# Kernel optimization log

Hardware: AMD Instinct MI355X
Metric: run time of the kernel (lower is better)

Reference implementation:

```python
import jax, jax.numpy as jnp
import numpy as np

N, K, D = 500_000, 256, 64  # points, prototypes, feature dim


def setup_inputs() -> dict:
    key = jax.random.key(0)
    kx, km = jax.random.split(key)
    X = jax.random.normal(kx, (N, D), dtype=jnp.float32)
    mus = jax.random.normal(km, (K, D), dtype=jnp.float32)
    return {"X": X, "mus": mus}


def reference(X, mus):
    # Faithful to vmap(lambda x: argmin(sum((mus - x)**2, axis=1)))(X),
    # but expressed with the Gram-matrix distance trick so the K*D broadcast
    # is a single GEMM instead of an O(N,K,D) elementwise intermediate.
    x_sq = jnp.sum(X * X, axis=1, keepdims=True)        # [N, 1]
    mu_sq = jnp.sum(mus * mus, axis=1)                  # [K]
    d2 = x_sq - 2.0 * (X @ mus.T) + mu_sq[None, :]      # [N, K] squared dists
    return jnp.argmin(d2, axis=1)                       # [N] int assignments
```

## Files before the change

kernel.cpp:

```cpp
#include <hip/hip_runtime.h>


#define DIM 64
#define NPROTO 256
#define NBLK 512
#define GSZ 16
#define MARGIN_ACC 0.017f

using f32x4 = __attribute__((ext_vector_type(4))) float;
using f16x8 = __attribute__((ext_vector_type(8))) _Float16;

__device__ __forceinline__ f16x8 cvt8(float4 a, float4 b) {
    f16x8 r;
    r[0] = (_Float16)a.x; r[1] = (_Float16)a.y;
    r[2] = (_Float16)a.z; r[3] = (_Float16)a.w;
    r[4] = (_Float16)b.x; r[5] = (_Float16)b.y;
    r[6] = (_Float16)b.z; r[7] = (_Float16)b.w;
    return r;
}

__attribute__((amdgpu_waves_per_eu(2, 4)))
__global__ void __launch_bounds__(256)
argmin_mfma_kernel(const float* __restrict__ X,
                   const float* __restrict__ mus,
                   int* __restrict__ out,
                   unsigned* __restrict__ ws_count,
                   int* __restrict__ ws_list,
                   int use_list, int n) {
    __shared__ __align__(16) float s_seed[NPROTO];

    const int tid = threadIdx.x;
    const int w = tid >> 6;
    const int l = tid & 63;
    const int lp = l & 15;
    const int lg = l >> 4;

    f16x8 ah[16][2];
#pragma unroll
    for (int p = 0; p < 16; ++p) {
        const float* src = mus + (size_t)(p * 16 + lp) * DIM + lg * 8;
        const float4 a = *(const float4*)(src);
        const float4 b = *(const float4*)(src + 4);
        const float4 c = *(const float4*)(src + 32);
        const float4 d = *(const float4*)(src + 36);
        ah[p][0] = cvt8(a, b);
        ah[p][1] = cvt8(c, d);
        float s = 0.f;
        s = fmaf(a.x, a.x, fmaf(a.y, a.y, fmaf(a.z, a.z, fmaf(a.w, a.w, s))));
        s = fmaf(b.x, b.x, fmaf(b.y, b.y, fmaf(b.z, b.z, fmaf(b.w, b.w, s))));
        s = fmaf(c.x, c.x, fmaf(c.y, c.y, fmaf(c.z, c.z, fmaf(c.w, c.w, s))));
        s = fmaf(d.x, d.x, fmaf(d.y, d.y, fmaf(d.z, d.z, fmaf(d.w, d.w, s))));
        s += __shfl_xor(s, 16);
        s += __shfl_xor(s, 32);
        if (w == 0 && lg == 0) s_seed[p * 16 + lp] = -0.5f * s;
    }
    __syncthreads();

    const int ngroups = (n + GSZ - 1) / GSZ;
    const int NW = NBLK * 4;
    const int gwid = blockIdx.x * 4 + w;
    const int q = ngroups / NW, rr = ngroups % NW;
    const int g0 = gwid * q + (gwid < rr ? gwid : rr);
    const int cnt = q + (gwid < rr ? 1 : 0);

    const int kofs = 255 - lg * 4;

    float4 xr0, xr1, xr2, xr3;
    if (cnt > 0) {
        int row = g0 * GSZ + lp; row = (row < n) ? row : (n - 1);
        const float* rp = X + (size_t)row * DIM + lg * 8;
        xr0 = *(const float4*)(rp);
        xr1 = *(const float4*)(rp + 4);
        xr2 = *(const float4*)(rp + 32);
        xr3 = *(const float4*)(rp + 36);
    }

    for (int it = 0; it < cnt; ++it) {
        const int g = g0 + it;
        const bool more = (it + 1 < cnt);

        const f16x8 bx0 = cvt8(xr0, xr1);
        const f16x8 bx1 = cvt8(xr2, xr3);

        if (more) {
            int row = (g + 1) * GSZ + lp; row = (row < n) ? row : (n - 1);
            const float* rp = X + (size_t)row * DIM + lg * 8;
            xr0 = *(const float4*)(rp);
            xr1 = *(const float4*)(rp + 4);
            xr2 = *(const float4*)(rp + 32);
            xr3 = *(const float4*)(rp + 36);
        }

        float b1 = -3.4e38f, b2 = -3.4e38f;
#pragma unroll
        for (int p = 0; p < 16; ++p) {
            const f32x4 seed = *(const f32x4*)&s_seed[p * 16 + lg * 4];
            f32x4 acc = __builtin_amdgcn_mfma_f32_16x16x32_f16(
                ah[p][0], bx0, seed, 0, 0, 0);
            acc = __builtin_amdgcn_mfma_f32_16x16x32_f16(ah[p][1], bx1, acc,
                                                         0, 0, 0);
            float pv[4];
#pragma unroll
            for (int r = 0; r < 4; ++r) {
                unsigned u = __float_as_uint(acc[r]);
                u = (u & 0xFFFFFF00u) + (unsigned)(kofs - p * 16 - r);
                pv[r] = __uint_as_float(u);
            }
            const float t1a = fmaxf(pv[0], pv[1]), t2a = fminf(pv[0], pv[1]);
            const float t1b = fmaxf(pv[2], pv[3]), t2b = fminf(pv[2], pv[3]);
            const float p1 = fmaxf(t1a, t1b);
            const float p2 = fmaxf(fminf(t1a, t1b), fmaxf(t2a, t2b));
            const float nb2 = fmaxf(fminf(b1, p1), fmaxf(b2, p2));
            b1 = fmaxf(b1, p1);
            b2 = nb2;
        }
#pragma unroll
        for (int m = 16; m <= 32; m <<= 1) {
            const float o1 = __shfl_xor(b1, m);
            const float o2 = __shfl_xor(b2, m);
            const float nb2 = fmaxf(fminf(b1, o1), fmaxf(b2, o2));
            b1 = fmaxf(b1, o1);
            b2 = nb2;
        }

        bool fl = false;
        const int i = g * GSZ + l;
        if (l < GSZ && i < n) {
            const unsigned u1 = __float_as_uint(b1);
            const int k1 = 255 - (int)(u1 & 0xFFu);
            const float f1 = __uint_as_float(u1 & 0xFFFFFF00u);
            const float f2 =
                __uint_as_float(__float_as_uint(b2) & 0xFFFFFF00u);
            const bool close = (f1 - f2) < MARGIN_ACC;
            if (use_list) {
                out[i] = k1;
                fl = close;
            } else {
                out[i] = (int)((unsigned)k1 | (close ? 0x80000000u : 0u));
            }
        }
        if (use_list) {
            const unsigned long long mask = __ballot(fl);
            if (mask) {
                unsigned base = 0;
                if (l == 0)
                    base = atomicAdd(ws_count, (unsigned)__popcll(mask));
                base = __shfl(base, 0);
                if (fl)
                    ws_list[base + __popcll(mask & ((1ull << l) - 1))] = i;
            }
        }
    }
}

#define MSTRIDE 65

__global__ void __launch_bounds__(256)
fixup_lds_kernel(const float* __restrict__ X, const float* __restrict__ mus,
                 const unsigned* __restrict__ ws_count,
                 const int* __restrict__ ws_list, int* __restrict__ out) {
    __shared__ float s_mu[NPROTO * MSTRIDE];
    __shared__ float s_msq[NPROTO];

    const int tid = threadIdx.x;
    {
        const float4* mr = (const float4*)(mus + (size_t)tid * DIM);
        float q0 = 0.f, q1 = 0.f, q2 = 0.f, q3 = 0.f;
#pragma unroll
        for (int qq = 0; qq < 16; ++qq) {
            const float4 mv = mr[qq];
            const int base = tid * MSTRIDE + qq * 4;
            s_mu[base]     = mv.x;
            s_mu[base + 1] = mv.y;
            s_mu[base + 2] = mv.z;
            s_mu[base + 3] = mv.w;
            q0 = fmaf(mv.x, mv.x, q0);
            q1 = fmaf(mv.y, mv.y, q1);
            q2 = fmaf(mv.z, mv.z, q2);
            q3 = fmaf(mv.w, mv.w, q3);
        }
        s_msq[tid] = (q0 + q1) + (q2 + q3);
    }
    __syncthreads();

    const int l = tid & 63;
    const int gw = (int)((blockIdx.x * blockDim.x + tid) >> 6);
    const int NW = (int)((gridDim.x * blockDim.x) >> 6);
    const int nf = (int)*ws_count;

    for (int j = gw; j < nf; j += NW) {
        const int pt = ws_list[j];
        const float4* xr = (const float4*)(X + (size_t)pt * DIM);
        float4 xv[16];
        float a0 = 0.f, a1 = 0.f, a2 = 0.f, a3 = 0.f;
#pragma unroll
        for (int qq = 0; qq < 16; ++qq) {
            xv[qq] = xr[qq];
            a0 = fmaf(xv[qq].x, xv[qq].x, a0);
            a1 = fmaf(xv[qq].y, xv[qq].y, a1);
            a2 = fmaf(xv[qq].z, xv[qq].z, a2);
            a3 = fmaf(xv[qq].w, xv[qq].w, a3);
        }
        const float xsq = (a0 + a1) + (a2 + a3);
        float b1 = 3.4e38f;
        int k1 = 0;
#pragma unroll
        for (int e = 0; e < 4; ++e) {
            const int p = e * 64 + l;
            const float* mr = &s_mu[p * MSTRIDE];
            float d0 = 0.f, d1 = 0.f, d2 = 0.f, d3 = 0.f;
#pragma unroll
            for (int qq = 0; qq < 16; ++qq) {
                d0 = fmaf(mr[qq * 4],     xv[qq].x, d0);
                d1 = fmaf(mr[qq * 4 + 1], xv[qq].y, d1);
                d2 = fmaf(mr[qq * 4 + 2], xv[qq].z, d2);
                d3 = fmaf(mr[qq * 4 + 3], xv[qq].w, d3);
            }
            const float dot = (d0 + d1) + (d2 + d3);
            const float dd = (xsq - 2.0f * dot) + s_msq[p];
            if (dd < b1) { b1 = dd; k1 = p; }
        }
#pragma unroll
        for (int mm = 1; mm < 64; mm <<= 1) {
            const float ob = __shfl_xor(b1, mm);
            const int ok = __shfl_xor(k1, mm);
            if (ob < b1 || (ob == b1 && ok < k1)) { b1 = ob; k1 = ok; }
        }
        if (l == 0) out[pt] = k1;
    }
}

__device__ __forceinline__ int recompute_point(const float* __restrict__ X,
                                               const float* __restrict__ mus,
                                               int pt, int l) {
    const float4* xr = (const float4*)(X + (size_t)pt * DIM);
    float4 xv[16];
    float xa0 = 0.f, xa1 = 0.f, xa2 = 0.f, xa3 = 0.f;
#pragma unroll
    for (int qq = 0; qq < 16; ++qq) {
        xv[qq] = xr[qq];
        xa0 = fmaf(xv[qq].x, xv[qq].x, xa0);
        xa1 = fmaf(xv[qq].y, xv[qq].y, xa1);
        xa2 = fmaf(xv[qq].z, xv[qq].z, xa2);
        xa3 = fmaf(xv[qq].w, xv[qq].w, xa3);
    }
    const float xsq = (xa0 + xa1) + (xa2 + xa3);
    float b1 = 3.4e38f; int k1 = 0;
#pragma unroll
    for (int e = 0; e < 4; ++e) {
        const int p = l * 4 + e;
        const float4* mr = (const float4*)(mus + (size_t)p * DIM);
        float d0 = 0.f, d1 = 0.f, d2a = 0.f, d3 = 0.f;
        float q0 = 0.f, q1 = 0.f, q2 = 0.f, q3 = 0.f;
#pragma unroll
        for (int qq = 0; qq < 16; ++qq) {
            const float4 mv = mr[qq];
            d0 = fmaf(mv.x, xv[qq].x, d0);
            d1 = fmaf(mv.y, xv[qq].y, d1);
            d2a = fmaf(mv.z, xv[qq].z, d2a);
            d3 = fmaf(mv.w, xv[qq].w, d3);
            q0 = fmaf(mv.x, mv.x, q0);
            q1 = fmaf(mv.y, mv.y, q1);
            q2 = fmaf(mv.z, mv.z, q2);
            q3 = fmaf(mv.w, mv.w, q3);
        }
        const float dot = (d0 + d1) + (d2a + d3);
        const float msq = (q0 + q1) + (q2 + q3);
        const float dd = (xsq - 2.0f * dot) + msq;
        if (dd < b1) { b1 = dd; k1 = p; }
    }
#pragma unroll
    for (int mm = 1; mm < 64; mm <<= 1) {
        const float ob = __shfl_xor(b1, mm);
        const int ok = __shfl_xor(k1, mm);
        if (ob < b1 || (ob == b1 && ok < k1)) { b1 = ob; k1 = ok; }
    }
    return k1;
}

__global__ void __launch_bounds__(256)
fixup_scan_kernel(const float* __restrict__ X, const float* __restrict__ mus,
                  int* __restrict__ out, int n) {
    const int gw = (int)((blockIdx.x * blockDim.x + threadIdx.x) >> 6);
    const int l = threadIdx.x & 63;
    const int NW = (int)((gridDim.x * blockDim.x) >> 6);
    const int chunk = (n + NW - 1) / NW;
    const int base = gw * chunk;
    const int end = (base + chunk < n) ? (base + chunk) : n;
    for (int s = base; s < end; s += 64) {
        const int i = s + l;
        const int v = (i < end) ? out[i] : 0;
        const bool flg = (i < end) && ((unsigned)v & 0x80000000u);
        unsigned long long m = __ballot(flg);
        while (m) {
            const int src = (int)__ffsll((unsigned long long)m) - 1;
            m &= m - 1;
            const int pt = __shfl(i, src);
            const int k1 = recompute_point(X, mus, pt, l);
            if (l == 0) out[pt] = k1;
        }
    }
}

extern "C" void kernel_launch(void* const* d_in, const int* in_sizes, int n_in,
                              void* d_out, int out_size, void* d_ws, size_t ws_size,
                              hipStream_t stream) {
    const float* X = (const float*)d_in[0];
    const float* mus = (const float*)d_in[1];
    int* out = (int*)d_out;
    const int n = in_sizes[0] / DIM;

    unsigned* ws_count = (unsigned*)d_ws;
    int* ws_list = (int*)((char*)d_ws + 16);
    const int use_list = (ws_size >= 16 + (size_t)n * 4) ? 1 : 0;

    if (use_list) {
        hipMemsetAsync(d_ws, 0, 16, stream);
    }

    argmin_mfma_kernel<<<NBLK, 256, 0, stream>>>(X, mus, out, ws_count,
                                                 ws_list, use_list, n);
    if (use_list) {
        fixup_lds_kernel<<<512, 256, 0, stream>>>(X, mus, ws_count, ws_list,
                                                  out);
    } else {
        fixup_scan_kernel<<<512, 256, 0, stream>>>(X, mus, out, n);
    }
}
```

Before: 89.73 us.

## Split prototypes across two waves and process two point tiles per iteration

Blocks shrink to two waves. Each wave now holds only 128 of the prototypes in registers instead of all 256, and it processes 32 points per iteration as two 16-point MFMA tiles. The two waves exchange their partial top-2 results through LDS behind a custom barrier that waits only on LDS and leaves outstanding global prefetches in flight. This halves per-wave register pressure for the prototype fragments and raises MFMA independence, which can help occupancy and latency hiding. In exchange it adds a block barrier on every iteration and a cross-wave LDS merge.

```diff
diff --git a/kernel.cpp b/kernel.cpp
--- a/kernel.cpp
+++ b/kernel.cpp
@@ -3,8 +3,7 @@
 
 #define DIM 64
 #define NPROTO 256
-#define NBLK 512
-#define GSZ 16
+#define NBLK 1024
 #define MARGIN_ACC 0.017f
 
 using f32x4 = __attribute__((ext_vector_type(4))) float;
@@ -19,8 +18,32 @@
     return r;
 }
 
+__device__ __forceinline__ void barrier_keep_vmcnt() {
+    asm volatile("s_waitcnt lgkmcnt(0)" ::: "memory");
+    __builtin_amdgcn_s_barrier();
+    __builtin_amdgcn_sched_barrier(0);
+}
+
+#define PACK_TREE(acc, b1, b2)                                          \
+    {                                                                   \
+        float pv[4];                                                    \
+        _Pragma("unroll")                                               \
+        for (int r = 0; r < 4; ++r) {                                   \
+            unsigned u = __float_as_uint(acc[r]);                       \
+            u = (u & 0xFFFFFF00u) + (unsigned)(kofs - p * 16 - r);      \
+            pv[r] = __uint_as_float(u);                                 \
+        }                                                               \
+        const float t1a = fmaxf(pv[0], pv[1]), t2a = fminf(pv[0], pv[1]);\
+        const float t1b = fmaxf(pv[2], pv[3]), t2b = fminf(pv[2], pv[3]);\
+        const float p1 = fmaxf(t1a, t1b);                               \
+        const float p2 = fmaxf(fminf(t1a, t1b), fmaxf(t2a, t2b));       \
+        const float nb2 = fmaxf(fminf(b1, p1), fmaxf(b2, p2));          \
+        b1 = fmaxf(b1, p1);                                             \
+        b2 = nb2;                                                       \
+    }
+
 __attribute__((amdgpu_waves_per_eu(2, 4)))
-__global__ void __launch_bounds__(256)
+__global__ void __launch_bounds__(128)
 argmin_mfma_kernel(const float* __restrict__ X,
                    const float* __restrict__ mus,
                    int* __restrict__ out,
@@ -28,6 +51,7 @@
                    int* __restrict__ ws_list,
                    int use_list, int n) {
     __shared__ __align__(16) float s_seed[NPROTO];
+    __shared__ uint2 s_pair[2][32];
 
     const int tid = threadIdx.x;
     const int w = tid >> 6;
@@ -35,10 +59,10 @@
     const int lp = l & 15;
     const int lg = l >> 4;
 
-    f16x8 ah[16][2];
-#pragma unroll
-    for (int p = 0; p < 16; ++p) {
-        const float* src = mus + (size_t)(p * 16 + lp) * DIM + lg * 8;
+    f16x8 ah[8][2];
+#pragma unroll
+    for (int p = 0; p < 8; ++p) {
+        const float* src = mus + (size_t)(w * 128 + p * 16 + lp) * DIM + lg * 8;
         const float4 a = *(const float4*)(src);
         const float4 b = *(const float4*)(src + 4);
         const float4 c = *(const float4*)(src + 32);
@@ -52,86 +76,99 @@
         s = fmaf(d.x, d.x, fmaf(d.y, d.y, fmaf(d.z, d.z, fmaf(d.w, d.w, s))));
         s += __shfl_xor(s, 16);
         s += __shfl_xor(s, 32);
-        if (w == 0 && lg == 0) s_seed[p * 16 + lp] = -0.5f * s;
+        if (lg == 0) s_seed[w * 128 + p * 16 + lp] = -0.5f * s;
     }
     __syncthreads();
 
-    const int ngroups = (n + GSZ - 1) / GSZ;
-    const int NW = NBLK * 4;
-    const int gwid = blockIdx.x * 4 + w;
-    const int q = ngroups / NW, rr = ngroups % NW;
-    const int g0 = gwid * q + (gwid < rr ? gwid : rr);
-    const int cnt = q + (gwid < rr ? 1 : 0);
-
-    const int kofs = 255 - lg * 4;
-
-    float4 xr0, xr1, xr2, xr3;
+    const int ng2 = (n + 31) / 32;
+    const int q = ng2 / NBLK, rr = ng2 % NBLK;
+    const int bid = blockIdx.x;
+    const int g0 = bid * q + (bid < rr ? bid : rr);
+    const int cnt = q + (bid < rr ? 1 : 0);
+
+    const int kofs = 255 - w * 128 - lg * 4;
+    const int sbase = w * 128 + lg * 4;
+
+    float4 xa0, xa1, xa2, xa3, xb0, xb1, xb2, xb3;
     if (cnt > 0) {
-        int row = g0 * GSZ + lp; row = (row < n) ? row : (n - 1);
-        const float* rp = X + (size_t)row * DIM + lg * 8;
-        xr0 = *(const float4*)(rp);
-        xr1 = *(const float4*)(rp + 4);
-        xr2 = *(const float4*)(rp + 32);
-        xr3 = *(const float4*)(rp + 36);
+        int rA = g0 * 32 + lp;      rA = (rA < n) ? rA : (n - 1);
+        int rB = g0 * 32 + 16 + lp; rB = (rB < n) ? rB : (n - 1);
+        const float* pA = X + (size_t)rA * DIM + lg * 8;
+        const float* pB = X + (size_t)rB * DIM + lg * 8;
+        xa0 = *(const float4*)(pA);      xa1 = *(const float4*)(pA + 4);
+        xa2 = *(const float4*)(pA + 32); xa3 = *(const float4*)(pA + 36);
+        xb0 = *(const float4*)(pB);      xb1 = *(const float4*)(pB + 4);
+        xb2 = *(const float4*)(pB + 32); xb3 = *(const float4*)(pB + 36);
     }
 
     for (int it = 0; it < cnt; ++it) {
         const int g = g0 + it;
+        const int par = it & 1;
         const bool more = (it + 1 < cnt);
 
-        const f16x8 bx0 = cvt8(xr0, xr1);
-        const f16x8 bx1 = cvt8(xr2, xr3);
+        const f16x8 bxA0 = cvt8(xa0, xa1), bxA1 = cvt8(xa2, xa3);
+        const f16x8 bxB0 = cvt8(xb0, xb1), bxB1 = cvt8(xb2, xb3);
 
         if (more) {
-            int row = (g + 1) * GSZ + lp; row = (row < n) ? row : (n - 1);
-            const float* rp = X + (size_t)row * DIM + lg * 8;
-            xr0 = *(const float4*)(rp);
-            xr1 = *(const float4*)(rp + 4);
-            xr2 = *(const float4*)(rp + 32);
-            xr3 = *(const float4*)(rp + 36);
-        }
-
-        float b1 = -3.4e38f, b2 = -3.4e38f;
-#pragma unroll
-        for (int p = 0; p < 16; ++p) {
-            const f32x4 seed = *(const f32x4*)&s_seed[p * 16 + lg * 4];
-            f32x4 acc = __builtin_amdgcn_mfma_f32_16x16x32_f16(
-                ah[p][0], bx0, seed, 0, 0, 0);
-            acc = __builtin_amdgcn_mfma_f32_16x16x32_f16(ah[p][1], bx1, acc,
-                                                         0, 0, 0);
-            float pv[4];
-#pragma unroll
-            for (int r = 0; r < 4; ++r) {
-                unsigned u = __float_as_uint(acc[r]);
-                u = (u & 0xFFFFFF00u) + (unsigned)(kofs - p * 16 - r);
-                pv[r] = __uint_as_float(u);
-            }
-            const float t1a = fmaxf(pv[0], pv[1]), t2a = fminf(pv[0], pv[1]);
-            const float t1b = fmaxf(pv[2], pv[3]), t2b = fminf(pv[2], pv[3]);
-            const float p1 = fmaxf(t1a, t1b);
-            const float p2 = fmaxf(fminf(t1a, t1b), fmaxf(t2a, t2b));
-            const float nb2 = fmaxf(fminf(b1, p1), fmaxf(b2, p2));
-            b1 = fmaxf(b1, p1);
-            b2 = nb2;
+            int rA = (g + 1) * 32 + lp;      rA = (rA < n) ? rA : (n - 1);
+            int rB = (g + 1) * 32 + 16 + lp; rB = (rB < n) ? rB : (n - 1);
+            const float* pA = X + (size_t)rA * DIM + lg * 8;
+            const float* pB = X + (size_t)rB * DIM + lg * 8;
+            xa0 = *(const float4*)(pA);      xa1 = *(const float4*)(pA + 4);
+            xa2 = *(const float4*)(pA + 32); xa3 = *(const float4*)(pA + 36);
+            xb0 = *(const float4*)(pB);      xb1 = *(const float4*)(pB + 4);
+            xb2 = *(const float4*)(pB + 32); xb3 = *(const float4*)(pB + 36);
+        }
+
+        float b1A = -3.4e38f, b2A = -3.4e38f;
+        float b1B = -3.4e38f, b2B = -3.4e38f;
+#pragma unroll
+        for (int p = 0; p < 8; ++p) {
+            const f32x4 seed = *(const f32x4*)&s_seed[sbase + p * 16];
+            f32x4 accA = __builtin_amdgcn_mfma_f32_16x16x32_f16(
+                ah[p][0], bxA0, seed, 0, 0, 0);
+            f32x4 accB = __builtin_amdgcn_mfma_f32_16x16x32_f16(
+                ah[p][0], bxB0, seed, 0, 0, 0);
+            accA = __builtin_amdgcn_mfma_f32_16x16x32_f16(ah[p][1], bxA1,
+                                                          accA, 0, 0, 0);
+            accB = __builtin_amdgcn_mfma_f32_16x16x32_f16(ah[p][1], bxB1,
+                                                          accB, 0, 0, 0);
+            PACK_TREE(accA, b1A, b2A)
+            PACK_TREE(accB, b1B, b2B)
         }
 #pragma unroll
         for (int m = 16; m <= 32; m <<= 1) {
-            const float o1 = __shfl_xor(b1, m);
-            const float o2 = __shfl_xor(b2, m);
-            const float nb2 = fmaxf(fminf(b1, o1), fmaxf(b2, o2));
-            b1 = fmaxf(b1, o1);
-            b2 = nb2;
-        }
+            const float o1A = __shfl_xor(b1A, m), o2A = __shfl_xor(b2A, m);
+            const float o1B = __shfl_xor(b1B, m), o2B = __shfl_xor(b2B, m);
+            const float n2A = fmaxf(fminf(b1A, o1A), fmaxf(b2A, o2A));
+            const float n2B = fmaxf(fminf(b1B, o1B), fmaxf(b2B, o2B));
+            b1A = fmaxf(b1A, o1A); b2A = n2A;
+            b1B = fmaxf(b1B, o1B); b2B = n2B;
+        }
+        if (w == 1 && l < 16) {
+            s_pair[par][l] = make_uint2(__float_as_uint(b1A),
+                                        __float_as_uint(b2A));
+            s_pair[par][16 + l] = make_uint2(__float_as_uint(b1B),
+                                             __float_as_uint(b2B));
+        }
+        barrier_keep_vmcnt();
 
         bool fl = false;
-        const int i = g * GSZ + l;
-        if (l < GSZ && i < n) {
-            const unsigned u1 = __float_as_uint(b1);
+        const int i = g * 32 + l;
+        if (w == 0 && l < 32 && i < n) {
+            float f1 = (l < 16) ? b1A : b1B;
+            float f2 = (l < 16) ? b2A : b2B;
+            const uint2 o = s_pair[par][l];
+            const float o1 = __uint_as_float(o.x), o2 = __uint_as_float(o.y);
+            const float nb2 = fmaxf(fminf(f1, o1), fmaxf(f2, o2));
+            f1 = fmaxf(f1, o1);
+            f2 = nb2;
+            const unsigned u1 = __float_as_uint(f1);
             const int k1 = 255 - (int)(u1 & 0xFFu);
-            const float f1 = __uint_as_float(u1 & 0xFFFFFF00u);
-            const float f2 =
-                __uint_as_float(__float_as_uint(b2) & 0xFFFFFF00u);
-            const bool close = (f1 - f2) < MARGIN_ACC;
+            const float v1 = __uint_as_float(u1 & 0xFFFFFF00u);
+            const float v2 =
+                __uint_as_float(__float_as_uint(f2) & 0xFFFFFF00u);
+            const bool close = (v1 - v2) < MARGIN_ACC;
             if (use_list) {
                 out[i] = k1;
                 fl = close;
@@ -318,7 +355,7 @@
         hipMemsetAsync(d_ws, 0, 16, stream);
     }
 
-    argmin_mfma_kernel<<<NBLK, 256, 0, stream>>>(X, mus, out, ws_count,
+    argmin_mfma_kernel<<<NBLK, 128, 0, stream>>>(X, mus, out, ws_count,
                                                  ws_list, use_list, n);
     if (use_list) {
         fixup_lds_kernel<<<512, 256, 0, stream>>>(X, mus, ws_count, ws_list,
```

New measurement: 77.28 us. 1.16x faster.

## Move prototype MFMA fragments to LDS, double grid and raise occupancy

Applied to the files above, without the earlier changes.

The main kernel no longer keeps all 32 f16x8 prototype fragments in registers. Each wave converts a quarter of them into shared memory once, and every group iteration reads its fragments from there. This frees many VGPRs, so the waves-per-EU hint rises to 4-8 and the grid doubles to 1024 blocks, giving more latency hiding. The non-list fallback fixup path now also stages prototypes in LDS. The cost is extra LDS reads in the inner loop, which may contend with the MFMAs.

```diff
diff --git a/kernel.cpp b/kernel.cpp
--- a/kernel.cpp
+++ b/kernel.cpp
@@ -3,8 +3,7 @@
 
 #define DIM 64
 #define NPROTO 256
-#define NBLK 512
-#define GSZ 16
+#define NBLK 1024
 #define MARGIN_ACC 0.017f
 
 using f32x4 = __attribute__((ext_vector_type(4))) float;
@@ -19,7 +18,7 @@
     return r;
 }
 
-__attribute__((amdgpu_waves_per_eu(2, 4)))
+__attribute__((amdgpu_waves_per_eu(4, 8)))
 __global__ void __launch_bounds__(256)
 argmin_mfma_kernel(const float* __restrict__ X,
                    const float* __restrict__ mus,
@@ -27,6 +26,7 @@
                    unsigned* __restrict__ ws_count,
                    int* __restrict__ ws_list,
                    int use_list, int n) {
+    __shared__ __align__(16) f16x8 s_frag[16][2][64];
     __shared__ __align__(16) float s_seed[NPROTO];
 
     const int tid = threadIdx.x;
@@ -35,16 +35,16 @@
     const int lp = l & 15;
     const int lg = l >> 4;
 
-    f16x8 ah[16][2];
-#pragma unroll
-    for (int p = 0; p < 16; ++p) {
+#pragma unroll
+    for (int pp = 0; pp < 4; ++pp) {
+        const int p = w * 4 + pp;
         const float* src = mus + (size_t)(p * 16 + lp) * DIM + lg * 8;
         const float4 a = *(const float4*)(src);
         const float4 b = *(const float4*)(src + 4);
         const float4 c = *(const float4*)(src + 32);
         const float4 d = *(const float4*)(src + 36);
-        ah[p][0] = cvt8(a, b);
-        ah[p][1] = cvt8(c, d);
+        s_frag[p][0][l] = cvt8(a, b);
+        s_frag[p][1][l] = cvt8(c, d);
         float s = 0.f;
         s = fmaf(a.x, a.x, fmaf(a.y, a.y, fmaf(a.z, a.z, fmaf(a.w, a.w, s))));
         s = fmaf(b.x, b.x, fmaf(b.y, b.y, fmaf(b.z, b.z, fmaf(b.w, b.w, s))));
@@ -52,11 +52,11 @@
         s = fmaf(d.x, d.x, fmaf(d.y, d.y, fmaf(d.z, d.z, fmaf(d.w, d.w, s))));
         s += __shfl_xor(s, 16);
         s += __shfl_xor(s, 32);
-        if (w == 0 && lg == 0) s_seed[p * 16 + lp] = -0.5f * s;
+        if (lg == 0) s_seed[p * 16 + lp] = -0.5f * s;
     }
     __syncthreads();
 
-    const int ngroups = (n + GSZ - 1) / GSZ;
+    const int ngroups = (n + 15) / 16;
     const int NW = NBLK * 4;
     const int gwid = blockIdx.x * 4 + w;
     const int q = ngroups / NW, rr = ngroups % NW;
@@ -67,7 +67,7 @@
 
     float4 xr0, xr1, xr2, xr3;
     if (cnt > 0) {
-        int row = g0 * GSZ + lp; row = (row < n) ? row : (n - 1);
+        int row = g0 * 16 + lp; row = (row < n) ? row : (n - 1);
         const float* rp = X + (size_t)row * DIM + lg * 8;
         xr0 = *(const float4*)(rp);
         xr1 = *(const float4*)(rp + 4);
@@ -83,7 +83,7 @@
         const f16x8 bx1 = cvt8(xr2, xr3);
 
         if (more) {
-            int row = (g + 1) * GSZ + lp; row = (row < n) ? row : (n - 1);
+            int row = (g + 1) * 16 + lp; row = (row < n) ? row : (n - 1);
             const float* rp = X + (size_t)row * DIM + lg * 8;
             xr0 = *(const float4*)(rp);
             xr1 = *(const float4*)(rp + 4);
@@ -94,10 +94,12 @@
         float b1 = -3.4e38f, b2 = -3.4e38f;
 #pragma unroll
         for (int p = 0; p < 16; ++p) {
+            const f16x8 A0 = s_frag[p][0][l];
+            const f16x8 A1 = s_frag[p][1][l];
             const f32x4 seed = *(const f32x4*)&s_seed[p * 16 + lg * 4];
             f32x4 acc = __builtin_amdgcn_mfma_f32_16x16x32_f16(
-                ah[p][0], bx0, seed, 0, 0, 0);
-            acc = __builtin_amdgcn_mfma_f32_16x16x32_f16(ah[p][1], bx1, acc,
+                A0, bx0, seed, 0, 0, 0);
+            acc = __builtin_amdgcn_mfma_f32_16x16x32_f16(A1, bx1, acc,
                                                          0, 0, 0);
             float pv[4];
 #pragma unroll
@@ -124,14 +126,14 @@
         }
 
         bool fl = false;
-        const int i = g * GSZ + l;
-        if (l < GSZ && i < n) {
+        const int i = g * 16 + l;
+        if (l < 16 && i < n) {
             const unsigned u1 = __float_as_uint(b1);
             const int k1 = 255 - (int)(u1 & 0xFFu);
-            const float f1 = __uint_as_float(u1 & 0xFFFFFF00u);
-            const float f2 =
+            const float v1 = __uint_as_float(u1 & 0xFFFFFF00u);
+            const float v2 =
                 __uint_as_float(__float_as_uint(b2) & 0xFFFFFF00u);
-            const bool close = (f1 - f2) < MARGIN_ACC;
+            const bool close = (v1 - v2) < MARGIN_ACC;
             if (use_list) {
                 out[i] = k1;
                 fl = close;
@@ -230,63 +232,41 @@
     }
 }
 
-__device__ __forceinline__ int recompute_point(const float* __restrict__ X,
-                                               const float* __restrict__ mus,
-                                               int pt, int l) {
-    const float4* xr = (const float4*)(X + (size_t)pt * DIM);
-    float4 xv[16];
-    float xa0 = 0.f, xa1 = 0.f, xa2 = 0.f, xa3 = 0.f;
-#pragma unroll
-    for (int qq = 0; qq < 16; ++qq) {
-        xv[qq] = xr[qq];
-        xa0 = fmaf(xv[qq].x, xv[qq].x, xa0);
-        xa1 = fmaf(xv[qq].y, xv[qq].y, xa1);
-        xa2 = fmaf(xv[qq].z, xv[qq].z, xa2);
-        xa3 = fmaf(xv[qq].w, xv[qq].w, xa3);
-    }
-    const float xsq = (xa0 + xa1) + (xa2 + xa3);
-    float b1 = 3.4e38f; int k1 = 0;
-#pragma unroll
-    for (int e = 0; e < 4; ++e) {
-        const int p = l * 4 + e;
-        const float4* mr = (const float4*)(mus + (size_t)p * DIM);
-        float d0 = 0.f, d1 = 0.f, d2a = 0.f, d3 = 0.f;
+__global__ void __launch_bounds__(256)
+fixup_scan_lds_kernel(const float* __restrict__ X,
+                      const float* __restrict__ mus,
+                      int* __restrict__ out, int n) {
+    __shared__ float s_mu[NPROTO * MSTRIDE];
+    __shared__ float s_msq[NPROTO];
+
+    const int tid = threadIdx.x;
+    {
+        const float4* mr = (const float4*)(mus + (size_t)tid * DIM);
         float q0 = 0.f, q1 = 0.f, q2 = 0.f, q3 = 0.f;
 #pragma unroll
         for (int qq = 0; qq < 16; ++qq) {
             const float4 mv = mr[qq];
-            d0 = fmaf(mv.x, xv[qq].x, d0);
-            d1 = fmaf(mv.y, xv[qq].y, d1);
-            d2a = fmaf(mv.z, xv[qq].z, d2a);
-            d3 = fmaf(mv.w, xv[qq].w, d3);
+            const int base = tid * MSTRIDE + qq * 4;
+            s_mu[base]     = mv.x;
+            s_mu[base + 1] = mv.y;
+            s_mu[base + 2] = mv.z;
+            s_mu[base + 3] = mv.w;
             q0 = fmaf(mv.x, mv.x, q0);
             q1 = fmaf(mv.y, mv.y, q1);
             q2 = fmaf(mv.z, mv.z, q2);
             q3 = fmaf(mv.w, mv.w, q3);
         }
-        const float dot = (d0 + d1) + (d2a + d3);
-        const float msq = (q0 + q1) + (q2 + q3);
-        const float dd = (xsq - 2.0f * dot) + msq;
-        if (dd < b1) { b1 = dd; k1 = p; }
-    }
-#pragma unroll
-    for (int mm = 1; mm < 64; mm <<= 1) {
-        const float ob = __shfl_xor(b1, mm);
-        const int ok = __shfl_xor(k1, mm);
-        if (ob < b1 || (ob == b1 && ok < k1)) { b1 = ob; k1 = ok; }
-    }
-    return k1;
-}
-
-__global__ void __launch_bounds__(256)
-fixup_scan_kernel(const float* __restrict__ X, const float* __restrict__ mus,
-                  int* __restrict__ out, int n) {
-    const int gw = (int)((blockIdx.x * blockDim.x + threadIdx.x) >> 6);
-    const int l = threadIdx.x & 63;
+        s_msq[tid] = (q0 + q1) + (q2 + q3);
+    }
+    __syncthreads();
+
+    const int l = tid & 63;
+    const int gw = (int)((blockIdx.x * blockDim.x + tid) >> 6);
     const int NW = (int)((gridDim.x * blockDim.x) >> 6);
     const int chunk = (n + NW - 1) / NW;
     const int base = gw * chunk;
     const int end = (base + chunk < n) ? (base + chunk) : n;
+
     for (int s = base; s < end; s += 64) {
         const int i = s + l;
         const int v = (i < end) ? out[i] : 0;
@@ -296,7 +276,42 @@
             const int src = (int)__ffsll((unsigned long long)m) - 1;
             m &= m - 1;
             const int pt = __shfl(i, src);
-            const int k1 = recompute_point(X, mus, pt, l);
+            const float4* xr = (const float4*)(X + (size_t)pt * DIM);
+            float4 xv[16];
+            float a0 = 0.f, a1 = 0.f, a2 = 0.f, a3 = 0.f;
+#pragma unroll
+            for (int qq = 0; qq < 16; ++qq) {
+                xv[qq] = xr[qq];
+                a0 = fmaf(xv[qq].x, xv[qq].x, a0);
+                a1 = fmaf(xv[qq].y, xv[qq].y, a1);
+                a2 = fmaf(xv[qq].z, xv[qq].z, a2);
+                a3 = fmaf(xv[qq].w, xv[qq].w, a3);
+            }
+            const float xsq = (a0 + a1) + (a2 + a3);
+            float b1 = 3.4e38f;
+            int k1 = 0;
+#pragma unroll
+            for (int e = 0; e < 4; ++e) {
+                const int p = e * 64 + l;
+                const float* mr = &s_mu[p * MSTRIDE];
+                float d0 = 0.f, d1 = 0.f, d2 = 0.f, d3 = 0.f;
+#pragma unroll
+                for (int qq = 0; qq < 16; ++qq) {
+                    d0 = fmaf(mr[qq * 4],     xv[qq].x, d0);
+                    d1 = fmaf(mr[qq * 4 + 1], xv[qq].y, d1);
+                    d2 = fmaf(mr[qq * 4 + 2], xv[qq].z, d2);
+                    d3 = fmaf(mr[qq * 4 + 3], xv[qq].w, d3);
+                }
+                const float dot = (d0 + d1) + (d2 + d3);
+                const float dd = (xsq - 2.0f * dot) + s_msq[p];
+                if (dd < b1) { b1 = dd; k1 = p; }
+            }
+#pragma unroll
+            for (int mm = 1; mm < 64; mm <<= 1) {
+                const float ob = __shfl_xor(b1, mm);
+                const int ok = __shfl_xor(k1, mm);
+                if (ob < b1 || (ob == b1 && ok < k1)) { b1 = ob; k1 = ok; }
+            }
             if (l == 0) out[pt] = k1;
         }
     }
@@ -324,6 +339,6 @@
         fixup_lds_kernel<<<512, 256, 0, stream>>>(X, mus, ws_count, ws_list,
                                                   out);
     } else {
-        fixup_scan_kernel<<<512, 256, 0, stream>>>(X, mus, out, n);
-    }
-}
+        fixup_scan_lds_kernel<<<512, 256, 0, stream>>>(X, mus, out, n);
+    }
+}
```

Measured after the change: 201.6 us. 125% more time.
